# Performance work log

Measured on AMD Instinct MI355X. Metric: run time of the kernel, lower is better.

Reference implementation:

```python
import jax, jax.numpy as jnp
import numpy as np
from jax import lax

B, C_IN, C_OUT, H, W, E = 16, 256, 256, 32, 32, 8


def setup_inputs() -> dict:
    key = jax.random.key(0)
    k = jax.random.split(key, 5)
    x = jax.random.normal(k[0], (B, C_IN, H, W), dtype=jnp.float32)
    # router: Conv2d(C_IN, E, kernel_size=1) -> weight [E, C_IN], bias [E]
    wc = jax.random.normal(k[1], (E, C_IN), dtype=jnp.float32) / np.sqrt(C_IN)
    bc = jnp.zeros((E,), dtype=jnp.float32)
    # experts: E x Conv2d(C_IN, C_OUT, 3, padding=1) + ReLU
    we = jax.random.normal(k[2], (E, C_OUT, C_IN, 3, 3), dtype=jnp.float32) / np.sqrt(C_IN * 9)
    be = jnp.zeros((E, C_OUT), dtype=jnp.float32)
    return {"x": x, "wc": wc, "bc": bc, "we": we, "be": be}


def reference(x, wc, bc, we, be):
    Bx = x.shape[0]
    # controller: 1x1 conv then global avg-pool == pool then linear
    pooled = jnp.mean(x, axis=(2, 3))                      # [B, C_IN]
    logits = pooled @ wc.T + bc                            # [B, E]
    decisions = jnp.argmax(logits, axis=1)                 # [B] int
    # run ALL experts on the full batch as one grouped conv: weight [E*C_OUT, C_IN, 3, 3]
    w_all = we.reshape(E * C_OUT, C_IN, 3, 3)
    y = lax.conv_general_dilated(
        x, w_all, window_strides=(1, 1), padding="SAME",
        dimension_numbers=("NCHW", "OIHW", "NCHW"))        # [B, E*C_OUT, H, W]
    y = y + be.reshape(1, E * C_OUT, 1, 1)
    y = jax.nn.relu(y).reshape(Bx, E, C_OUT, H, W)
    # faithful to forward_test: out block i is components[dec[i]](x) for the FULL batch
    # out[i*B + j] = y[j, dec[i]]
    gathered = y[:, decisions]                             # [j, i, C_OUT, H, W]
    out = jnp.swapaxes(gathered, 0, 1).reshape(Bx * Bx, C_OUT, H, W)
    return out
```

## Files before the change

kernel.cpp:

```cpp
#include <hip/hip_runtime.h>
#include <hip/hip_bf16.h>
#include <stdint.h>

#define B_    16
#define CIN   256
#define COUT  256
#define E_    8
#define HW    1024
#define PH    34
#define PW    34

typedef __attribute__((ext_vector_type(8))) short  short8;
typedef __attribute__((ext_vector_type(4))) float  floatx4;

#define XT_OFF 17408
#define XT_BYTES (B_*PH*PW*CIN*2)
#define WT_OFF (XT_OFF + XT_BYTES)

__device__ __forceinline__ void gld_lds16(const void* g, void* l) {
    __builtin_amdgcn_global_load_lds(
        (const __attribute__((address_space(1))) unsigned int*)g,
        (__attribute__((address_space(3))) unsigned int*)l,
        16, 0, 0);
}

__global__ __launch_bounds__(256) void prep_kernel(
    const float* __restrict__ x, const float* __restrict__ we,
    unsigned short* __restrict__ xt, unsigned short* __restrict__ wt,
    float* __restrict__ pooled) {
    int bid = blockIdx.x;
    int t = threadIdx.x;
    if (bid < 128) {
        int b = bid >> 3, ci0 = (bid & 7) * 32;
        __shared__ float tileF[32][65];
        float psum[8];
        #pragma unroll
        for (int li = 0; li < 8; ++li) psum[li] = 0.0f;
        int hwl = t & 63, wv = t >> 6;
        int hwl2 = t >> 2, grp = t & 3;
        for (int chunk = 0; chunk < 16; ++chunk) {
            #pragma unroll
            for (int li = 0; li < 8; ++li) {
                int ci = wv + li*4;
                float v = x[((size_t)b*CIN + ci0 + ci)*HW + chunk*64 + hwl];
                tileF[ci][hwl] = v;
                psum[li] += v;
            }
            __syncthreads();
            int hw = chunk*64 + hwl2;
            int h = hw >> 5, w = hw & 31;
            short8 v8;
            #pragma unroll
            for (int q = 0; q < 8; ++q) {
                __hip_bfloat16 hv = __float2bfloat16(tileF[grp*8 + q][hwl2]);
                v8[q] = *(short*)&hv;
            }
            *(short8*)&xt[(((size_t)b*PH + h + 1)*PW + (w + 1))*CIN + ci0 + grp*8] = v8;
            __syncthreads();
        }
        #pragma unroll
        for (int li = 0; li < 8; ++li) {
            float s = psum[li];
            #pragma unroll
            for (int o = 32; o > 0; o >>= 1) s += __shfl_down(s, o, 64);
            if ((t & 63) == 0) pooled[b*CIN + ci0 + wv + li*4] = s;
        }
        short8 z = {0,0,0,0,0,0,0,0};
        for (int idx = t; idx < 528; idx += 256) {
            int pos = idx >> 2, sub = idx & 3;
            int h, w;
            if (pos < 34)       { h = 0;            w = pos; }
            else if (pos < 68)  { h = 33;           w = pos - 34; }
            else if (pos < 100) { h = pos - 68 + 1; w = 0; }
            else                { h = pos - 100 + 1;w = 33; }
            *(short8*)&xt[(((size_t)b*PH + h)*PW + w)*CIN + ci0 + sub*8] = z;
        }
    } else {
        int wbid = bid - 128;
        int e = wbid >> 8, co = wbid & 255;
        __shared__ float buf[CIN*9];
        const float* src = we + ((size_t)e*COUT + co)*CIN*9;
        #pragma unroll
        for (int k = 0; k < 9; ++k) buf[t + k*256] = src[t + k*256];
        __syncthreads();
        for (int idx = t; idx < 288; idx += 256) {
            int rs = idx >> 5, grp = idx & 31;
            short8 v;
            #pragma unroll
            for (int q = 0; q < 8; ++q) {
                __hip_bfloat16 h = __float2bfloat16(buf[(grp*8 + q)*9 + rs]);
                v[q] = *(short*)&h;
            }
            *(short8*)&wt[(((size_t)e*9 + rs)*COUT + co)*CIN + grp*8] = v;
        }
    }
}

__global__ __launch_bounds__(128) void decide_kernel(
    const float* __restrict__ pooled, const float* __restrict__ wc,
    const float* __restrict__ bc, int* __restrict__ dec) {
    int t = threadIdx.x;
    int b = t >> 3, e = t & 7;
    float acc = 0.0f;
    const float4* pp = (const float4*)(pooled + b*CIN);
    const float4* ww = (const float4*)(wc + e*CIN);
    #pragma unroll 4
    for (int i = 0; i < CIN/4; ++i) {
        float4 p = pp[i], w = ww[i];
        acc += p.x*w.x + p.y*w.y + p.z*w.z + p.w*w.w;
    }
    acc = acc * (1.0f/1024.0f) + bc[e];
    __shared__ float lg[16][8];
    lg[b][e] = acc;
    __syncthreads();
    if (e == 0) {
        float best = lg[b][0]; int bi = 0;
        #pragma unroll
        for (int j = 1; j < 8; ++j) { if (lg[b][j] > best) { best = lg[b][j]; bi = j; } }
        dec[b] = bi;
    }
}

__global__ __launch_bounds__(256) void conv_kernel(
    const unsigned short* __restrict__ xt, const unsigned short* __restrict__ wt,
    const float* __restrict__ be, const int* __restrict__ dec,
    float* __restrict__ out) {

    int tile = blockIdx.x;
    int b = blockIdx.y;
    int e = blockIdx.z;
    int mt = tile >> 3, nt = tile & 7;

    int dcs[16];
    #pragma unroll
    for (int i = 0; i < 16; ++i) dcs[i] = dec[i];
    bool active = false;
    #pragma unroll
    for (int i = 0; i < 16; ++i) active |= (dcs[i] == e);
    if (!active) return;

    __shared__ __align__(16) unsigned short sA[2][512*8];
    __shared__ __align__(16) unsigned short sB[832*8];

    int t = threadIdx.x;
    int wave = t >> 6, lane = t & 63;
    int wm = wave >> 1, wn = wave & 1;
    int kg = lane >> 4, ln = lane & 15;

    int ph0 = nt * 4;
    int co0 = mt * 128;

    floatx4 acc[4][4];
    #pragma unroll
    for (int i = 0; i < 4; ++i)
        #pragma unroll
        for (int j = 0; j < 4; ++j) acc[i][j] = (floatx4)0.0f;

    const unsigned short* xb = xt + ((size_t)b*PH + ph0)*PW*CIN;
    const unsigned short* wb = wt + (size_t)e*9*COUT*CIN + (size_t)co0*CIN;

    auto stageA = [&](int ck, int sh, int buf) {
        const unsigned short* wsrc = wb + (size_t)sh*COUT*CIN + ck*32;
        #pragma unroll
        for (int k = 0; k < 2; ++k) {
            int c = t + k*256;
            int row = c >> 2, gs = c & 3;
            int g = gs ^ ((row >> 1) & 3);
            gld_lds16(wsrc + (size_t)row*CIN + g*8, &sA[buf][c*8]);
        }
    };
    auto stageB = [&](int ck) {
        const unsigned short* xsrc = xb + ck*32;
        #pragma unroll
        for (int k = 0; k < 3; ++k) {
            int c = t + k*256;
            int rB = c >> 2, gs = c & 3;
            int g = gs ^ ((rB >> 1) & 3);
            gld_lds16(xsrc + (size_t)rB*CIN + g*8, &sB[c*8]);
        }
        if (t < 64) {
            int c = t + 768;
            int cc = c < 816 ? c : 815;
            int rB = cc >> 2, gs = cc & 3;
            int g = gs ^ ((rB >> 1) & 3);
            gld_lds16(xsrc + (size_t)rB*CIN + g*8, &sB[c*8]);
        }
    };

    short8 a[4], bv[4];
    auto readA = [&](int ab) {
        #pragma unroll
        for (int im = 0; im < 4; ++im) {
            int row = wm*64 + im*16 + ln;
            int cL = row*4 + (kg ^ ((row >> 1) & 3));
            a[im] = *(const short8*)(&sA[ab][cL*8]);
        }
    };
    auto readB = [&](int r, int s) {
        #pragma unroll
        for (int in = 0; in < 4; ++in) {
            int n  = wn*64 + in*16 + ln;
            int hl = n >> 5, wl = n & 31;
            int rB = (hl + r)*34 + (wl + s);
            int cL = rB*4 + (kg ^ ((rB >> 1) & 3));
            bv[in] = *(const short8*)(&sB[cL*8]);
        }
    };

    stageB(0);
    stageA(0, 0, 0);
    __syncthreads();

    for (int ck = 0; ck < 8; ++ck) {
        for (int sh = 0; sh < 9; ++sh) {
            int it = ck*9 + sh;
            int ab = it & 1;
            int r = sh / 3, s = sh - r*3;

            if (sh < 8) {
                stageA(ck, sh + 1, ab ^ 1);
                readA(ab);
                readB(r, s);
                #pragma unroll
                for (int im = 0; im < 4; ++im)
                    #pragma unroll
                    for (int in = 0; in < 4; ++in)
                        acc[im][in] = __builtin_amdgcn_mfma_f32_16x16x32_bf16(bv[in], a[im], acc[im][in], 0, 0, 0);
                __syncthreads();
            } else {
                readB(r, s);
                if (ck < 7) {
                    asm volatile("s_waitcnt lgkmcnt(0)" ::: "memory");
                    __builtin_amdgcn_s_barrier();
                    stageB(ck + 1);
                    stageA(ck + 1, 0, ab ^ 1);
                }
                readA(ab);
                #pragma unroll
                for (int im = 0; im < 4; ++im)
                    #pragma unroll
                    for (int in = 0; in < 4; ++in)
                        acc[im][in] = __builtin_amdgcn_mfma_f32_16x16x32_bf16(bv[in], a[im], acc[im][in], 0, 0, 0);
                if (ck < 7) __syncthreads();
            }
        }
    }

    float bias[4];
    #pragma unroll
    for (int im = 0; im < 4; ++im)
        bias[im] = be[e*COUT + co0 + wm*64 + im*16 + ln];
    #pragma unroll
    for (int im = 0; im < 4; ++im)
        #pragma unroll
        for (int in = 0; in < 4; ++in)
            #pragma unroll
            for (int rg = 0; rg < 4; ++rg) {
                float v = acc[im][in][rg] + bias[im];
                acc[im][in][rg] = v > 0.0f ? v : 0.0f;
            }

    for (int i = 0; i < 16; ++i) {
        if (dcs[i] != e) continue;
        float* ob = out + (size_t)(i*16 + b)*COUT*HW;
        #pragma unroll
        for (int im = 0; im < 4; ++im) {
            int co = co0 + wm*64 + im*16 + ln;
            float* orow = ob + (size_t)co*HW + nt*128 + wn*64 + kg*4;
            #pragma unroll
            for (int in = 0; in < 4; ++in)
                *(floatx4*)(orow + in*16) = acc[im][in];
        }
    }
}

extern "C" void kernel_launch(void* const* d_in, const int* in_sizes, int n_in,
                              void* d_out, int out_size, void* d_ws, size_t ws_size,
                              hipStream_t stream) {
    const float* x  = (const float*)d_in[0];
    const float* wc = (const float*)d_in[1];
    const float* bc = (const float*)d_in[2];
    const float* we = (const float*)d_in[3];
    const float* be = (const float*)d_in[4];
    float* out = (float*)d_out;

    char* ws = (char*)d_ws;
    int*   dec    = (int*)ws;
    float* pooled = (float*)(ws + 64);
    unsigned short* xt = (unsigned short*)(ws + XT_OFF);
    unsigned short* wt = (unsigned short*)(ws + WT_OFF);

    prep_kernel  <<<2176, 256, 0, stream>>>(x, we, xt, wt, pooled);
    decide_kernel<<<1, 128, 0, stream>>>(pooled, wc, bc, dec);
    conv_kernel  <<<dim3(16, 16, 8), 256, 0, stream>>>(xt, wt, be, dec, out);
}
```

Before: 464.0 us.

## Double the K chunk per stage and remap block ids across XCDs

The conv kernel now stages 64 input channels per chunk instead of 32, halving the number of chunk iterations and barriers per tile. The LDS swizzle is reworked for 8 groups per row, and each shift step runs two MFMA passes. The 3D grid is flattened to 1D with a remap that spreads consecutive block ids across the 8 XCDs while keeping tiles of the same batch and expert together for L2 reuse. Shared memory per block roughly doubles, which may lower occupancy.

```diff
diff --git a/kernel.cpp b/kernel.cpp
--- a/kernel.cpp
+++ b/kernel.cpp
@@ -126,9 +126,12 @@
     const float* __restrict__ be, const int* __restrict__ dec,
     float* __restrict__ out) {
 
-    int tile = blockIdx.x;
-    int b = blockIdx.y;
-    int e = blockIdx.z;
+    int gid = blockIdx.x;
+    int wid = (gid & 7) * 256 + (gid >> 3);
+    int tile = wid & 15;
+    int g_   = wid >> 4;
+    int e = g_ & 7;
+    int b = g_ >> 3;
     int mt = tile >> 3, nt = tile & 7;
 
     int dcs[16];
@@ -139,8 +142,8 @@
     for (int i = 0; i < 16; ++i) active |= (dcs[i] == e);
     if (!active) return;
 
-    __shared__ __align__(16) unsigned short sA[2][512*8];
-    __shared__ __align__(16) unsigned short sB[832*8];
+    __shared__ __align__(16) unsigned short sA[2][1024*8];
+    __shared__ __align__(16) unsigned short sB[1792*8];
 
     int t = threadIdx.x;
     int wave = t >> 6, lane = t & 63;
@@ -160,58 +163,61 @@
     const unsigned short* wb = wt + (size_t)e*9*COUT*CIN + (size_t)co0*CIN;
 
     auto stageA = [&](int ck, int sh, int buf) {
-        const unsigned short* wsrc = wb + (size_t)sh*COUT*CIN + ck*32;
-        #pragma unroll
-        for (int k = 0; k < 2; ++k) {
+        const unsigned short* wsrc = wb + (size_t)sh*COUT*CIN + ck*64;
+        #pragma unroll
+        for (int k = 0; k < 4; ++k) {
             int c = t + k*256;
-            int row = c >> 2, gs = c & 3;
-            int g = gs ^ ((row >> 1) & 3);
-            gld_lds16(wsrc + (size_t)row*CIN + g*8, &sA[buf][c*8]);
+            int row = c >> 3, gl = c & 7;
+            int gs = gl ^ (row & 7);
+            gld_lds16(wsrc + (size_t)row*CIN + gs*8, &sA[buf][c*8]);
         }
     };
     auto stageB = [&](int ck) {
-        const unsigned short* xsrc = xb + ck*32;
-        #pragma unroll
-        for (int k = 0; k < 3; ++k) {
+        const unsigned short* xsrc = xb + ck*64;
+        #pragma unroll
+        for (int k = 0; k < 7; ++k) {
             int c = t + k*256;
-            int rB = c >> 2, gs = c & 3;
-            int g = gs ^ ((rB >> 1) & 3);
-            gld_lds16(xsrc + (size_t)rB*CIN + g*8, &sB[c*8]);
-        }
-        if (t < 64) {
-            int c = t + 768;
-            int cc = c < 816 ? c : 815;
-            int rB = cc >> 2, gs = cc & 3;
-            int g = gs ^ ((rB >> 1) & 3);
-            gld_lds16(xsrc + (size_t)rB*CIN + g*8, &sB[c*8]);
+            int cc = c < 1632 ? c : 1631;
+            int rB = cc >> 3, gl = cc & 7;
+            int gs = gl ^ (rB & 7);
+            gld_lds16(xsrc + (size_t)rB*CIN + gs*8, &sB[c*8]);
         }
     };
 
     short8 a[4], bv[4];
-    auto readA = [&](int ab) {
+    auto readA = [&](int kh, int ab) {
         #pragma unroll
         for (int im = 0; im < 4; ++im) {
             int row = wm*64 + im*16 + ln;
-            int cL = row*4 + (kg ^ ((row >> 1) & 3));
+            int gl = kh*4 + kg;
+            int cL = row*8 + (gl ^ (row & 7));
             a[im] = *(const short8*)(&sA[ab][cL*8]);
         }
     };
-    auto readB = [&](int r, int s) {
+    auto readB = [&](int kh, int r, int s) {
         #pragma unroll
         for (int in = 0; in < 4; ++in) {
             int n  = wn*64 + in*16 + ln;
             int hl = n >> 5, wl = n & 31;
             int rB = (hl + r)*34 + (wl + s);
-            int cL = rB*4 + (kg ^ ((rB >> 1) & 3));
+            int gl = kh*4 + kg;
+            int cL = rB*8 + (gl ^ (rB & 7));
             bv[in] = *(const short8*)(&sB[cL*8]);
         }
+    };
+    auto mfma16 = [&]() {
+        #pragma unroll
+        for (int im = 0; im < 4; ++im)
+            #pragma unroll
+            for (int in = 0; in < 4; ++in)
+                acc[im][in] = __builtin_amdgcn_mfma_f32_16x16x32_bf16(bv[in], a[im], acc[im][in], 0, 0, 0);
     };
 
     stageB(0);
     stageA(0, 0, 0);
     __syncthreads();
 
-    for (int ck = 0; ck < 8; ++ck) {
+    for (int ck = 0; ck < 4; ++ck) {
         for (int sh = 0; sh < 9; ++sh) {
             int it = ck*9 + sh;
             int ab = it & 1;
@@ -219,29 +225,20 @@
 
             if (sh < 8) {
                 stageA(ck, sh + 1, ab ^ 1);
-                readA(ab);
-                readB(r, s);
-                #pragma unroll
-                for (int im = 0; im < 4; ++im)
-                    #pragma unroll
-                    for (int in = 0; in < 4; ++in)
-                        acc[im][in] = __builtin_amdgcn_mfma_f32_16x16x32_bf16(bv[in], a[im], acc[im][in], 0, 0, 0);
+                readA(0, ab); readB(0, r, s); mfma16();
+                readA(1, ab); readB(1, r, s); mfma16();
                 __syncthreads();
             } else {
-                readB(r, s);
-                if (ck < 7) {
+                readA(0, ab); readB(0, r, s); mfma16();
+                readB(1, r, s);
+                if (ck < 3) {
                     asm volatile("s_waitcnt lgkmcnt(0)" ::: "memory");
                     __builtin_amdgcn_s_barrier();
                     stageB(ck + 1);
                     stageA(ck + 1, 0, ab ^ 1);
                 }
-                readA(ab);
-                #pragma unroll
-                for (int im = 0; im < 4; ++im)
-                    #pragma unroll
-                    for (int in = 0; in < 4; ++in)
-                        acc[im][in] = __builtin_amdgcn_mfma_f32_16x16x32_bf16(bv[in], a[im], acc[im][in], 0, 0, 0);
-                if (ck < 7) __syncthreads();
+                readA(1, ab); mfma16();
+                if (ck < 3) __syncthreads();
             }
         }
     }
@@ -292,5 +289,5 @@
 
     prep_kernel  <<<2176, 256, 0, stream>>>(x, we, xt, wt, pooled);
     decide_kernel<<<1, 128, 0, stream>>>(pooled, wc, bc, dec);
-    conv_kernel  <<<dim3(16, 16, 8), 256, 0, stream>>>(xt, wt, be, dec, out);
-}
+    conv_kernel  <<<2048, 256, 0, stream>>>(xt, wt, be, dec, out);
+}
```

Result: faster. 434.7 us (-6.3%).
